# Kernel optimization log

Hardware: AMD Instinct MI355X
Metric: run time of the kernel (lower is better)

Reference implementation:

```python
import jax, jax.numpy as jnp
import numpy as np

N_NODES = 100000
N_EDGES = 1600000
N_FEAT = 128
HIDDEN = 128
OUT = 1
NUM_GRAPHS = 2048


def setup_inputs() -> dict:
    key = jax.random.key(0)
    ks = jax.random.split(key, 8)
    x = jax.random.normal(ks[0], (N_NODES, N_FEAT), dtype=jnp.float32)
    edge_index = jax.random.randint(ks[1], (2, N_EDGES), 0, N_NODES, dtype=jnp.int64)
    batch = jnp.sort(jax.random.randint(ks[2], (N_NODES,), 0, NUM_GRAPHS, dtype=jnp.int64))
    s = 1.0 / np.sqrt(N_FEAT)
    W1 = jax.random.normal(ks[3], (N_FEAT, HIDDEN), dtype=jnp.float32) * s
    b1 = jnp.zeros((HIDDEN,), dtype=jnp.float32)
    W2 = jax.random.normal(ks[4], (HIDDEN, HIDDEN), dtype=jnp.float32) * s
    b2 = jnp.zeros((HIDDEN,), dtype=jnp.float32)
    Wlin = jax.random.normal(ks[5], (HIDDEN, OUT), dtype=jnp.float32) * s
    blin = jnp.zeros((OUT,), dtype=jnp.float32)
    return {"x": x, "edge_index": edge_index, "batch": batch,
            "W1": W1, "b1": b1, "W2": W2, "b2": b2, "Wlin": Wlin, "blin": blin}


def gcn_conv(x, W, b, src, dst, n_nodes):
    # PyG GCNConv: x' = D^{-1/2} (A + I) D^{-1/2} (X W) + b, deg includes self-loop
    xw = x @ W  # [N, H]
    deg = jax.ops.segment_sum(jnp.ones(src.shape[0], xw.dtype), dst, num_segments=n_nodes) + 1.0
    dinv = jax.lax.rsqrt(deg)
    norm = dinv[src] * dinv[dst]  # [E]
    agg = jax.ops.segment_sum(xw[src] * norm[:, None], dst, num_segments=n_nodes)
    # self-loop contribution: norm = deg^{-1}
    return agg + xw * (1.0 / deg)[:, None] + b


def global_mean_pool(x, batch, num_graphs):
    sums = jax.ops.segment_sum(x, batch, num_segments=num_graphs)
    cnts = jax.ops.segment_sum(jnp.ones(x.shape[0], x.dtype), batch, num_segments=num_graphs)
    return sums / jnp.maximum(cnts, 1.0)[:, None]


def reference(x, edge_index, batch, W1, b1, W2, b2, Wlin, blin):
    src, dst = edge_index[0], edge_index[1]
    n = x.shape[0]
    h = gcn_conv(x, W1, b1, src, dst, n)
    h = jax.nn.relu(h)  # dropout is a no-op in eval mode
    h = gcn_conv(h, W2, b2, src, dst, n)
    g = global_mean_pool(h, batch, NUM_GRAPHS)  # [G, H]
    return g @ Wlin + blin
```

## Files before the change

### kernel.cpp

```cpp
#include <hip/hip_runtime.h>

#define N_NODES   100000
#define N_EDGES   1600000
#define NFEAT     128
#define NGRAPHS   2048
#define CBSHIFT   7
#define BSZ       128
#define NCB       ((N_NODES + BSZ - 1) / BSZ)
#define N_META    (NCB * BSZ)
#define CAP       2432
#define P1_EPB    4096
#define P1_BLOCKS ((N_EDGES + P1_EPB - 1) / P1_EPB)
#define GEMM_HALF   391
#define G1_BLOCKS 2048
#define G2_BLOCKS ((4 * N_NODES + 255) / 256)
#define ZCNT      (NGRAPHS + NCB)
#define ZB        ((ZCNT + 255) / 256)
#define MISC_BLOCKS (17 + ZB + 8)

typedef __attribute__((ext_vector_type(8))) short short8;
typedef __attribute__((ext_vector_type(4))) float f32x4;

__device__ __forceinline__ unsigned short f2bf(float f) {
    unsigned int u = __float_as_uint(f);
    u += 0x7FFFu + ((u >> 16) & 1u);
    return (unsigned short)(u >> 16);
}

__device__ __forceinline__ void acc8s(float* acc, uint4 v, float s) {
    acc[0] = fmaf(s, __uint_as_float(v.x << 16), acc[0]);
    acc[1] = fmaf(s, __uint_as_float(v.x & 0xFFFF0000u), acc[1]);
    acc[2] = fmaf(s, __uint_as_float(v.y << 16), acc[2]);
    acc[3] = fmaf(s, __uint_as_float(v.y & 0xFFFF0000u), acc[3]);
    acc[4] = fmaf(s, __uint_as_float(v.z << 16), acc[4]);
    acc[5] = fmaf(s, __uint_as_float(v.z & 0xFFFF0000u), acc[5]);
    acc[6] = fmaf(s, __uint_as_float(v.w << 16), acc[6]);
    acc[7] = fmaf(s, __uint_as_float(v.w & 0xFFFF0000u), acc[7]);
}

__device__ __forceinline__ void gemm_tile(const float* __restrict__ X,
                                          const unsigned short* __restrict__ WT,
                                          unsigned short* __restrict__ C,
                                          int gblk, int tid) {
    const int R0   = gblk * 128;
    const int wv   = tid >> 6;
    const int lane = tid & 63;
    const int m16  = lane & 15;
    const int quad = lane >> 4;
    const int r0 = R0 + wv * 32 + m16;
    const int r1 = r0 + 16;
    const bool ok0 = r0 < N_NODES, ok1 = r1 < N_NODES;

    f32x4 acc[2][8] = {};
    #pragma unroll
    for (int ks = 0; ks < 4; ++ks) {
        const int k0 = ks * 32 + quad * 8;
        short8 a0 = {}, a1 = {};
        if (ok0) {
            float4 f0 = *(const float4*)(X + (size_t)r0 * NFEAT + k0);
            float4 f1 = *(const float4*)(X + (size_t)r0 * NFEAT + k0 + 4);
            a0[0] = (short)f2bf(f0.x); a0[1] = (short)f2bf(f0.y);
            a0[2] = (short)f2bf(f0.z); a0[3] = (short)f2bf(f0.w);
            a0[4] = (short)f2bf(f1.x); a0[5] = (short)f2bf(f1.y);
            a0[6] = (short)f2bf(f1.z); a0[7] = (short)f2bf(f1.w);
        }
        if (ok1) {
            float4 f0 = *(const float4*)(X + (size_t)r1 * NFEAT + k0);
            float4 f1 = *(const float4*)(X + (size_t)r1 * NFEAT + k0 + 4);
            a1[0] = (short)f2bf(f0.x); a1[1] = (short)f2bf(f0.y);
            a1[2] = (short)f2bf(f0.z); a1[3] = (short)f2bf(f0.w);
            a1[4] = (short)f2bf(f1.x); a1[5] = (short)f2bf(f1.y);
            a1[6] = (short)f2bf(f1.z); a1[7] = (short)f2bf(f1.w);
        }
        #pragma unroll
        for (int ct = 0; ct < 8; ++ct) {
            short8 bb = *(const short8*)(WT + (ct * 16 + m16) * 128 + k0);
            acc[0][ct] = __builtin_amdgcn_mfma_f32_16x16x32_bf16(a0, bb, acc[0][ct], 0, 0, 0);
            acc[1][ct] = __builtin_amdgcn_mfma_f32_16x16x32_bf16(a1, bb, acc[1][ct], 0, 0, 0);
        }
    }
    #pragma unroll
    for (int t2 = 0; t2 < 2; ++t2) {
        int rbase = R0 + wv * 32 + t2 * 16 + quad * 4;
        #pragma unroll
        for (int reg = 0; reg < 4; ++reg) {
            int gr = rbase + reg;
            if (gr < N_NODES) {
                short8 v;
                #pragma unroll
                for (int ct = 0; ct < 8; ++ct)
                    v[ct] = (short)f2bf(acc[t2][ct][reg]);
                *(short8*)(C + (size_t)gr * NFEAT + m16 * 8) = v;
            }
        }
    }
}

__global__ __launch_bounds__(256) void k_misc(const float* __restrict__ W1,
                                              unsigned short* __restrict__ WT1,
                                              const float* __restrict__ W2,
                                              const float* __restrict__ Wlin,
                                              const float* __restrict__ b2,
                                              const float* __restrict__ blin,
                                              float* __restrict__ w2l,
                                              int* __restrict__ zeros,
                                              const int* __restrict__ batch,
                                              float* __restrict__ cntf) {
    const int blk = blockIdx.x;
    const int t = threadIdx.x;
    if (blk < 16) {
        int base = blk * 1024 + t * 4;
        #pragma unroll
        for (int q = 0; q < 4; ++q) {
            int i = base + q;
            int n = i >> 7, k = i & 127;
            WT1[i] = f2bf(W1[k * 128 + n]);
        }
    } else if (blk == 16) {
        __shared__ float s[256];
        int i = t >> 1, half = t & 1;
        float ps = 0.f;
        for (int j = half * 64; j < half * 64 + 64; ++j)
            ps += W2[i * 128 + j] * Wlin[j];
        s[t] = ps;
        __syncthreads();
        if (!half) w2l[i] = s[t] + s[t + 1];
        __syncthreads();
        float pc = (t < 128) ? b2[t] * Wlin[t] : 0.f;
        s[t] = pc;
        __syncthreads();
        for (int off = 128; off > 0; off >>= 1) {
            if (t < off) s[t] += s[t + off];
            __syncthreads();
        }
        if (t == 0) w2l[128] = s[0] + blin[0];
    } else if (blk < 17 + ZB) {
        int i = (blk - 17) * 256 + t;
        if (i < ZCNT) zeros[i] = 0;
    } else {
        int g = (blk - (17 + ZB)) * 256 + t;
        int lo = 0, hi = N_NODES;
        while (lo < hi) { int m = (lo + hi) >> 1; if (batch[m] < g) lo = m + 1; else hi = m; }
        int lb = lo;
        lo = 0; hi = N_NODES;
        int g1 = g + 1;
        while (lo < hi) { int m = (lo + hi) >> 1; if (batch[m] < g1) lo = m + 1; else hi = m; }
        cntf[g] = fmaxf((float)(lo - lb), 1.0f);
    }
}

__global__ __launch_bounds__(256) void k_gA_p1(const float* __restrict__ X,
                                               const unsigned short* __restrict__ WT,
                                               unsigned short* __restrict__ C,
                                               const int* __restrict__ src,
                                               const int* __restrict__ dst,
                                               int* __restrict__ bcur,
                                               unsigned int* __restrict__ pairs) {
    if (blockIdx.x < GEMM_HALF) {
        gemm_tile(X, WT, C, blockIdx.x, threadIdx.x);
        return;
    }
    const int b = blockIdx.x - GEMM_HALF;
    __shared__ int hist[NCB], base[NCB], cur[NCB];
    const int t = threadIdx.x;
    for (int i = t; i < NCB; i += 256) { hist[i] = 0; cur[i] = 0; }
    __syncthreads();
    const int e0 = b * P1_EPB;
    const int e1 = min(e0 + P1_EPB, N_EDGES);
    const int q0 = e0 >> 2, q1 = e1 >> 2;
    const int4* dst4 = (const int4*)dst;
    const int4* src4 = (const int4*)src;
    for (int q = q0 + t; q < q1; q += 256) {
        int4 d4 = dst4[q];
        atomicAdd(&hist[d4.x >> CBSHIFT], 1);
        atomicAdd(&hist[d4.y >> CBSHIFT], 1);
        atomicAdd(&hist[d4.z >> CBSHIFT], 1);
        atomicAdd(&hist[d4.w >> CBSHIFT], 1);
    }
    __syncthreads();
    const int off0 = (b * 89) % NCB;
    for (int k = t; k < NCB; k += 256) {
        int i = k + off0;
        if (i >= NCB) i -= NCB;
        int c = hist[i];
        base[i] = c ? (i * CAP + atomicAdd(&bcur[i], c)) : 0;
    }
    __syncthreads();
    for (int q = q0 + t; q < q1; q += 256) {
        int4 d4 = dst4[q];
        int4 s4 = src4[q];
        #pragma unroll
        for (int u = 0; u < 4; ++u) {
            int d = (u == 0) ? d4.x : (u == 1) ? d4.y : (u == 2) ? d4.z : d4.w;
            int sv = (u == 0) ? s4.x : (u == 1) ? s4.y : (u == 2) ? s4.z : s4.w;
            int bb = d >> CBSHIFT;
            int r = atomicAdd(&cur[bb], 1);
            int idx = base[bb] + r;
            if (idx < (bb + 1) * CAP)
                pairs[idx] = (unsigned int)sv | ((unsigned int)(d & (BSZ - 1)) << 17);
        }
    }
}

__global__ __launch_bounds__(256) void k_gB_p2(const float* __restrict__ X,
                                               const unsigned short* __restrict__ WT,
                                               unsigned short* __restrict__ C,
                                               const unsigned int* __restrict__ pairs,
                                               const int* __restrict__ bcur,
                                               int* __restrict__ csr_src,
                                               float* __restrict__ dinv,
                                               int4* __restrict__ meta,
                                               int2* __restrict__ nm) {
    if (blockIdx.x < GEMM_HALF) {
        gemm_tile(X, WT, C, blockIdx.x + GEMM_HALF, threadIdx.x);
        return;
    }
    const int b = blockIdx.x - GEMM_HALF;
    __shared__ int hist[BSZ], sst[BSZ], cur[BSZ], s[BSZ], dh[64], dhc[64];
    const int t = threadIdx.x;
    const int cnt_b = min(bcur[b], CAP);
    const int beg = b * CAP;
    const int end = beg + cnt_b;
    const int end4 = beg + (cnt_b & ~3);
    if (t < BSZ) { hist[t] = 0; cur[t] = 0; }
    if (t < 64) { dh[t] = 0; dhc[t] = 0; }
    __syncthreads();
    for (int i = beg + 4 * t; i < end4; i += 1024) {
        uint4 pv = *(const uint4*)(pairs + i);
        atomicAdd(&hist[pv.x >> 17], 1);
        atomicAdd(&hist[pv.y >> 17], 1);
        atomicAdd(&hist[pv.z >> 17], 1);
        atomicAdd(&hist[pv.w >> 17], 1);
    }
    for (int i = end4 + t; i < end; i += 256)
        atomicAdd(&hist[pairs[i] >> 17], 1);
    __syncthreads();
    int v = (t < BSZ) ? hist[t] : 0;
    if (t < BSZ) s[t] = v;
    __syncthreads();
    for (int off = 1; off < BSZ; off <<= 1) {
        int x = (t >= off && t < BSZ) ? s[t - off] : 0;
        __syncthreads();
        if (t < BSZ) s[t] += x;
        __syncthreads();
    }
    if (t < BSZ) sst[t] = s[t] - v;
    __syncthreads();
    const int node = (b << CBSHIFT) + t;
    const bool valid = (t < BSZ) && (node < N_NODES);
    if (valid) {
        dinv[node] = rsqrtf((float)v + 1.0f);
        nm[node] = make_int2(beg + sst[t], v);
        atomicAdd(&dh[63 - min(v, 63)], 1);
    }
    for (int i = beg + 4 * t; i < end4; i += 1024) {
        uint4 pv = *(const uint4*)(pairs + i);
        #pragma unroll
        for (int u = 0; u < 4; ++u) {
            unsigned int p = (u == 0) ? pv.x : (u == 1) ? pv.y : (u == 2) ? pv.z : pv.w;
            int dl = p >> 17;
            int r = atomicAdd(&cur[dl], 1);
            csr_src[beg + sst[dl] + r] = (int)(p & 0x1FFFFu);
        }
    }
    for (int i = end4 + t; i < end; i += 256) {
        unsigned int pv = pairs[i];
        int dl = pv >> 17;
        int r = atomicAdd(&cur[dl], 1);
        csr_src[beg + sst[dl] + r] = (int)(pv & 0x1FFFFu);
    }
    __syncthreads();
    if (t < 64) s[t] = dh[t];
    __syncthreads();
    for (int off = 1; off < 64; off <<= 1) {
        int x = (t >= off && t < 64) ? s[t - off] : 0;
        __syncthreads();
        if (t < 64) s[t] += x;
        __syncthreads();
    }
    if (valid) {
        int bin = 63 - min(v, 63);
        int r = atomicAdd(&dhc[bin], 1);
        int rank = s[bin] - dh[bin] + r;
        meta[(size_t)rank * NCB + b] =
            make_int4(beg + sst[t], v, __float_as_int(rsqrtf((float)v + 1.0f)), node);
    } else if (t < BSZ) {
        meta[(size_t)t * NCB + b] = make_int4(0, 0, 0, -1);
    }
}

__global__ __launch_bounds__(256) void k_gather1(const unsigned short* __restrict__ xwb,
                                                 const int* __restrict__ csr_src,
                                                 const float* __restrict__ dinv,
                                                 const float* __restrict__ b,
                                                 const float* __restrict__ w2l,
                                                 const int4* __restrict__ meta,
                                                 float* __restrict__ z) {
    const int t     = threadIdx.x;
    const int lane  = t & 63;
    const int p     = lane & 15;
    const int gbase = lane & 48;
    const int j0    = p & 7;
    const int ngroups = G1_BLOCKS * 16;
    int gid = blockIdx.x * 16 + (t >> 4);
    const uint4* tab = (const uint4*)xwb;
    float bl[8], wl[8];
    #pragma unroll
    for (int j = 0; j < 8; ++j) { bl[j] = b[16 * j + p]; wl[j] = w2l[16 * j + p]; }

    for (int nidx = gid; nidx < N_META; nidx += ngroups) {
        const int4 md = meta[nidx];
        const int node  = md.w;
        if (node < 0) continue;
        const int beg   = md.x;
        const int cnt   = md.y;
        const float dvn = __int_as_float(md.z);
        float acc[8] = {};
        acc8s(acc, tab[(size_t)node * 16 + p], dvn);
        const int nch = (cnt + 7) >> 3;
        if (nch) {
            int myA; float dvA; uint4 vA[8];
            int myB; float dvB; uint4 vB[8];
            {
                bool vld = j0 < cnt;
                int jj = vld ? j0 : 0;
                int sld = csr_src[beg + jj];
                myA = vld ? sld : node;
                float dv = dinv[myA];
                dvA = vld ? dv : 0.f;
                #pragma unroll
                for (int q = 0; q < 8; ++q) {
                    int idx = __shfl(myA, gbase + q);
                    vA[q] = tab[(size_t)idx * 16 + p];
                }
            }
            int c = 0;
            for (;;) {
                const bool hb = (c + 1 < nch);
                if (hb) {
                    int j = (c + 1) * 8 + j0;
                    bool vld = j < cnt;
                    int jj = vld ? j : 0;
                    int sld = csr_src[beg + jj];
                    myB = vld ? sld : node;
                    float dv = dinv[myB];
                    dvB = vld ? dv : 0.f;
                    #pragma unroll
                    for (int q = 0; q < 8; ++q) {
                        int idx = __shfl(myB, gbase + q);
                        vB[q] = tab[(size_t)idx * 16 + p];
                    }
                }
                #pragma unroll
                for (int q = 0; q < 8; ++q) {
                    float sv = __shfl(dvA, gbase + q);
                    acc8s(acc, vA[q], sv);
                }
                ++c;
                if (!hb) break;
                const bool ha = (c + 1 < nch);
                if (ha) {
                    int j = (c + 1) * 8 + j0;
                    bool vld = j < cnt;
                    int jj = vld ? j : 0;
                    int sld = csr_src[beg + jj];
                    myA = vld ? sld : node;
                    float dv = dinv[myA];
                    dvA = vld ? dv : 0.f;
                    #pragma unroll
                    for (int q = 0; q < 8; ++q) {
                        int idx = __shfl(myA, gbase + q);
                        vA[q] = tab[(size_t)idx * 16 + p];
                    }
                }
                #pragma unroll
                for (int q = 0; q < 8; ++q) {
                    float sv = __shfl(dvB, gbase + q);
                    acc8s(acc, vB[q], sv);
                }
                ++c;
                if (!ha) break;
            }
        }
        float s = 0.f;
        #pragma unroll
        for (int j = 0; j < 8; ++j)
            s = fmaf(fmaxf(fmaf(acc[j], dvn, bl[j]), 0.f), wl[j], s);
        s += __shfl_xor(s, 1);
        s += __shfl_xor(s, 2);
        s += __shfl_xor(s, 4);
        s += __shfl_xor(s, 8);
        if (p == 0) z[node] = s * dvn;
    }
}

__global__ __launch_bounds__(256) void k_g2(const float* __restrict__ z,
                                            const int* __restrict__ csr_src,
                                            const int2* __restrict__ nm,
                                            const float* __restrict__ dinv,
                                            const int* __restrict__ batch,
                                            float* __restrict__ gsum) {
    __shared__ float lgs[64];
    __shared__ int sg0;
    const int t = threadIdx.x;
    if (t < 64) lgs[t] = 0.f;
    const int node0 = blockIdx.x * 64;
    if (t == 0) sg0 = batch[node0];
    __syncthreads();
    const int g0 = sg0;
    const int node = node0 + (t >> 2);
    const int q = t & 3;
    if (node < N_NODES) {
        int2 m = nm[node];
        const int beg = m.x, cnt = m.y;
        float a = (q == 0) ? z[node] : 0.f;
        for (int j = q; j < cnt; j += 4)
            a += z[csr_src[beg + j]];
        a += __shfl_xor(a, 1);
        a += __shfl_xor(a, 2);
        if (q == 0) {
            float val = a * dinv[node];
            int rel = batch[node] - g0;
            if (rel < 64) atomicAdd(&lgs[rel], val);
            else atomicAdd(&gsum[batch[node]], val);
        }
    }
    __syncthreads();
    if (t < 64 && lgs[t] != 0.f) atomicAdd(&gsum[g0 + t], lgs[t]);
}

__global__ void k_final(const float* __restrict__ gsum, const float* __restrict__ cntf,
                        const float* __restrict__ c2, float* __restrict__ out) {
    int g = blockIdx.x * blockDim.x + threadIdx.x;
    if (g >= NGRAPHS) return;
    out[g] = gsum[g] / cntf[g] + c2[0];
}

extern "C" void kernel_launch(void* const* d_in, const int* in_sizes, int n_in,
                              void* d_out, int out_size, void* d_ws, size_t ws_size,
                              hipStream_t stream) {
    const float* x    = (const float*)d_in[0];
    const int*   ei   = (const int*)d_in[1];
    const int*   bat  = (const int*)d_in[2];
    const float* W1   = (const float*)d_in[3];
    const float* b1   = (const float*)d_in[4];
    const float* W2   = (const float*)d_in[5];
    const float* b2   = (const float*)d_in[6];
    const float* Wlin = (const float*)d_in[7];
    const float* blin = (const float*)d_in[8];
    float* out = (float*)d_out;

    const int* src = ei;
    const int* dst = ei + N_EDGES;

    const size_t NF = (size_t)N_NODES * NFEAT;
    unsigned short* bufA = (unsigned short*)d_ws;
    float* z       = (float*)(bufA + NF);
    float* dinv    = z + N_NODES;
    float* gsum    = dinv + N_NODES;
    int* bcur      = (int*)(gsum + NGRAPHS);
    float* cntf    = (float*)(bcur + NCB);
    unsigned short* WT1 = (unsigned short*)(cntf + NGRAPHS);
    float* w2l     = (float*)(WT1 + 128 * 128);
    unsigned int* pairs = (unsigned int*)(w2l + 132);
    int* csr_src   = (int*)(pairs + (size_t)NCB * CAP);
    int4* meta     = (int4*)(((size_t)(csr_src + (size_t)NCB * CAP) + 15) & ~(size_t)15);
    int2* nm       = (int2*)(meta + N_META);

    const int BS = 256;

    k_misc<<<MISC_BLOCKS, BS, 0, stream>>>(W1, WT1, W2, Wlin, b2, blin, w2l,
                                           (int*)gsum, bat, cntf);
    k_gA_p1<<<GEMM_HALF + P1_BLOCKS, BS, 0, stream>>>(x, WT1, bufA, src, dst, bcur, pairs);
    k_gB_p2<<<GEMM_HALF + NCB, BS, 0, stream>>>(x, WT1, bufA, pairs, bcur, csr_src,
                                                dinv, meta, nm);
    k_gather1<<<G1_BLOCKS, BS, 0, stream>>>(bufA, csr_src, dinv, b1, w2l, meta, z);
    k_g2<<<G2_BLOCKS, BS, 0, stream>>>(z, csr_src, nm, dinv, bat, gsum);
    k_final<<<(NGRAPHS + BS - 1) / BS, BS, 0, stream>>>(gsum, cntf, w2l + 128, out);
}
```

Measured before the change: 228.9 us.

## Fuse CSR bucket scatter into layer-1 gather with LDS-resident CSR

The CSR scatter and degree-ordered rank metadata move out of the GEMM/degree kernel into a new per-bucket kernel. That kernel builds the bucket's CSR slice in shared memory, sorts its nodes by degree locally, and immediately runs the layer-1 gather from the LDS copy. This removes the global meta array and the reread of csr_src in the gather. The cost is that gather parallelism is now tied to one block per 128-node bucket, which may hurt load balance compared with the old global degree-sorted grid-stride schedule. Shared-memory use per block also rises, which may lower occupancy.

```diff
diff --git a/kernel.cpp b/kernel.cpp
--- a/kernel.cpp
+++ b/kernel.cpp
@@ -7,12 +7,10 @@
 #define CBSHIFT   7
 #define BSZ       128
 #define NCB       ((N_NODES + BSZ - 1) / BSZ)
-#define N_META    (NCB * BSZ)
 #define CAP       2432
 #define P1_EPB    4096
 #define P1_BLOCKS ((N_EDGES + P1_EPB - 1) / P1_EPB)
 #define GEMM_HALF   391
-#define G1_BLOCKS 2048
 #define G2_BLOCKS ((4 * N_NODES + 255) / 256)
 #define ZCNT      (NGRAPHS + NCB)
 #define ZB        ((ZCNT + 255) / 256)
@@ -202,28 +200,25 @@
     }
 }
 
-__global__ __launch_bounds__(256) void k_gB_p2(const float* __restrict__ X,
-                                               const unsigned short* __restrict__ WT,
-                                               unsigned short* __restrict__ C,
-                                               const unsigned int* __restrict__ pairs,
-                                               const int* __restrict__ bcur,
-                                               int* __restrict__ csr_src,
-                                               float* __restrict__ dinv,
-                                               int4* __restrict__ meta,
-                                               int2* __restrict__ nm) {
+__global__ __launch_bounds__(256) void k_gB_deg(const float* __restrict__ X,
+                                                const unsigned short* __restrict__ WT,
+                                                unsigned short* __restrict__ C,
+                                                const unsigned int* __restrict__ pairs,
+                                                const int* __restrict__ bcur,
+                                                int2* __restrict__ nm,
+                                                float* __restrict__ dinv) {
     if (blockIdx.x < GEMM_HALF) {
         gemm_tile(X, WT, C, blockIdx.x + GEMM_HALF, threadIdx.x);
         return;
     }
     const int b = blockIdx.x - GEMM_HALF;
-    __shared__ int hist[BSZ], sst[BSZ], cur[BSZ], s[BSZ], dh[64], dhc[64];
+    __shared__ int hist[BSZ], s[BSZ];
     const int t = threadIdx.x;
     const int cnt_b = min(bcur[b], CAP);
     const int beg = b * CAP;
     const int end = beg + cnt_b;
     const int end4 = beg + (cnt_b & ~3);
-    if (t < BSZ) { hist[t] = 0; cur[t] = 0; }
-    if (t < 64) { dh[t] = 0; dhc[t] = 0; }
+    if (t < BSZ) hist[t] = 0;
     __syncthreads();
     for (int i = beg + 4 * t; i < end4; i += 1024) {
         uint4 pv = *(const uint4*)(pairs + i);
@@ -244,77 +239,89 @@
         if (t < BSZ) s[t] += x;
         __syncthreads();
     }
-    if (t < BSZ) sst[t] = s[t] - v;
-    __syncthreads();
     const int node = (b << CBSHIFT) + t;
-    const bool valid = (t < BSZ) && (node < N_NODES);
+    if (t < BSZ && node < N_NODES) {
+        nm[node] = make_int2(beg + s[t] - v, v);
+        dinv[node] = rsqrtf((float)v + 1.0f);
+    }
+}
+
+__global__ __launch_bounds__(256) void k_bg(const unsigned short* __restrict__ xwb,
+                                            const unsigned int* __restrict__ pairs,
+                                            const int* __restrict__ bcur,
+                                            const int2* __restrict__ nm,
+                                            const float* __restrict__ dinv,
+                                            const float* __restrict__ b,
+                                            const float* __restrict__ w2l,
+                                            int* __restrict__ csr_src,
+                                            float* __restrict__ z) {
+    __shared__ int csr_lds[CAP];
+    __shared__ int begL[BSZ], cntL[BSZ], cur[BSZ];
+    __shared__ float dvL[BSZ];
+    __shared__ int dh[64], dhc[64], s64[64];
+    __shared__ unsigned char rankord[BSZ];
+    const int bb = blockIdx.x;
+    const int t = threadIdx.x;
+    const int node0 = bb << CBSHIFT;
+    if (t < BSZ) {
+        int node = node0 + t;
+        cur[t] = 0;
+        rankord[t] = 255;
+        if (node < N_NODES) {
+            int2 m = nm[node];
+            begL[t] = m.x - bb * CAP;
+            cntL[t] = m.y;
+            dvL[t] = dinv[node];
+        } else { begL[t] = 0; cntL[t] = 0; dvL[t] = 0.f; }
+    }
+    if (t < 64) { dh[t] = 0; dhc[t] = 0; }
+    __syncthreads();
+    const bool valid = (t < BSZ) && (node0 + t < N_NODES);
+    int bin = 0;
+    if (valid) { bin = 63 - min(cntL[t], 63); atomicAdd(&dh[bin], 1); }
+    __syncthreads();
+    if (t < 64) s64[t] = dh[t];
+    __syncthreads();
+    for (int off = 1; off < 64; off <<= 1) {
+        int x = (t >= off && t < 64) ? s64[t - off] : 0;
+        __syncthreads();
+        if (t < 64) s64[t] += x;
+        __syncthreads();
+    }
     if (valid) {
-        dinv[node] = rsqrtf((float)v + 1.0f);
-        nm[node] = make_int2(beg + sst[t], v);
-        atomicAdd(&dh[63 - min(v, 63)], 1);
-    }
-    for (int i = beg + 4 * t; i < end4; i += 1024) {
-        uint4 pv = *(const uint4*)(pairs + i);
-        #pragma unroll
-        for (int u = 0; u < 4; ++u) {
-            unsigned int p = (u == 0) ? pv.x : (u == 1) ? pv.y : (u == 2) ? pv.z : pv.w;
-            int dl = p >> 17;
-            int r = atomicAdd(&cur[dl], 1);
-            csr_src[beg + sst[dl] + r] = (int)(p & 0x1FFFFu);
-        }
-    }
-    for (int i = end4 + t; i < end; i += 256) {
-        unsigned int pv = pairs[i];
+        int r = atomicAdd(&dhc[bin], 1);
+        rankord[s64[bin] - dh[bin] + r] = (unsigned char)t;
+    }
+    const int cnt_b = min(bcur[bb], CAP);
+    const int pbase = bb * CAP;
+    __syncthreads();
+    for (int i = t; i < cnt_b; i += 256) {
+        unsigned int pv = pairs[pbase + i];
         int dl = pv >> 17;
         int r = atomicAdd(&cur[dl], 1);
-        csr_src[beg + sst[dl] + r] = (int)(pv & 0x1FFFFu);
-    }
-    __syncthreads();
-    if (t < 64) s[t] = dh[t];
-    __syncthreads();
-    for (int off = 1; off < 64; off <<= 1) {
-        int x = (t >= off && t < 64) ? s[t - off] : 0;
-        __syncthreads();
-        if (t < 64) s[t] += x;
-        __syncthreads();
-    }
-    if (valid) {
-        int bin = 63 - min(v, 63);
-        int r = atomicAdd(&dhc[bin], 1);
-        int rank = s[bin] - dh[bin] + r;
-        meta[(size_t)rank * NCB + b] =
-            make_int4(beg + sst[t], v, __float_as_int(rsqrtf((float)v + 1.0f)), node);
-    } else if (t < BSZ) {
-        meta[(size_t)t * NCB + b] = make_int4(0, 0, 0, -1);
-    }
-}
-
-__global__ __launch_bounds__(256) void k_gather1(const unsigned short* __restrict__ xwb,
-                                                 const int* __restrict__ csr_src,
-                                                 const float* __restrict__ dinv,
-                                                 const float* __restrict__ b,
-                                                 const float* __restrict__ w2l,
-                                                 const int4* __restrict__ meta,
-                                                 float* __restrict__ z) {
-    const int t     = threadIdx.x;
+        int idx = begL[dl] + r;
+        int sv = (int)(pv & 0x1FFFFu);
+        csr_lds[idx] = sv;
+        csr_src[pbase + idx] = sv;
+    }
+    __syncthreads();
     const int lane  = t & 63;
     const int p     = lane & 15;
     const int gbase = lane & 48;
     const int j0    = p & 7;
-    const int ngroups = G1_BLOCKS * 16;
-    int gid = blockIdx.x * 16 + (t >> 4);
+    const int grp   = t >> 4;
     const uint4* tab = (const uint4*)xwb;
     float bl[8], wl[8];
     #pragma unroll
     for (int j = 0; j < 8; ++j) { bl[j] = b[16 * j + p]; wl[j] = w2l[16 * j + p]; }
 
-    for (int nidx = gid; nidx < N_META; nidx += ngroups) {
-        const int4 md = meta[nidx];
-        const int node  = md.w;
-        if (node < 0) continue;
-        const int beg   = md.x;
-        const int cnt   = md.y;
-        const float dvn = __int_as_float(md.z);
+    for (int r = grp; r < BSZ; r += 16) {
+        const int tl = rankord[r];
+        if (tl == 255) continue;
+        const int node  = node0 + tl;
+        const int begl  = begL[tl];
+        const int cnt   = cntL[tl];
+        const float dvn = dvL[tl];
         float acc[8] = {};
         acc8s(acc, tab[(size_t)node * 16 + p], dvn);
         const int nch = (cnt + 7) >> 3;
@@ -324,7 +331,7 @@
             {
                 bool vld = j0 < cnt;
                 int jj = vld ? j0 : 0;
-                int sld = csr_src[beg + jj];
+                int sld = csr_lds[begl + jj];
                 myA = vld ? sld : node;
                 float dv = dinv[myA];
                 dvA = vld ? dv : 0.f;
@@ -341,7 +348,7 @@
                     int j = (c + 1) * 8 + j0;
                     bool vld = j < cnt;
                     int jj = vld ? j : 0;
-                    int sld = csr_src[beg + jj];
+                    int sld = csr_lds[begl + jj];
                     myB = vld ? sld : node;
                     float dv = dinv[myB];
                     dvB = vld ? dv : 0.f;
@@ -363,7 +370,7 @@
                     int j = (c + 1) * 8 + j0;
                     bool vld = j < cnt;
                     int jj = vld ? j : 0;
-                    int sld = csr_src[beg + jj];
+                    int sld = csr_lds[begl + jj];
                     myA = vld ? sld : node;
                     float dv = dinv[myA];
                     dvA = vld ? dv : 0.f;
@@ -464,17 +471,15 @@
     float* w2l     = (float*)(WT1 + 128 * 128);
     unsigned int* pairs = (unsigned int*)(w2l + 132);
     int* csr_src   = (int*)(pairs + (size_t)NCB * CAP);
-    int4* meta     = (int4*)(((size_t)(csr_src + (size_t)NCB * CAP) + 15) & ~(size_t)15);
-    int2* nm       = (int2*)(meta + N_META);
+    int2* nm       = (int2*)(csr_src + (size_t)NCB * CAP);
 
     const int BS = 256;
 
     k_misc<<<MISC_BLOCKS, BS, 0, stream>>>(W1, WT1, W2, Wlin, b2, blin, w2l,
                                            (int*)gsum, bat, cntf);
     k_gA_p1<<<GEMM_HALF + P1_BLOCKS, BS, 0, stream>>>(x, WT1, bufA, src, dst, bcur, pairs);
-    k_gB_p2<<<GEMM_HALF + NCB, BS, 0, stream>>>(x, WT1, bufA, pairs, bcur, csr_src,
-                                                dinv, meta, nm);
-    k_gather1<<<G1_BLOCKS, BS, 0, stream>>>(bufA, csr_src, dinv, b1, w2l, meta, z);
+    k_gB_deg<<<GEMM_HALF + NCB, BS, 0, stream>>>(x, WT1, bufA, pairs, bcur, nm, dinv);
+    k_bg<<<NCB, BS, 0, stream>>>(bufA, pairs, bcur, nm, dinv, b1, w2l, csr_src, z);
     k_g2<<<G2_BLOCKS, BS, 0, stream>>>(z, csr_src, nm, dinv, bat, gsum);
     k_final<<<(NGRAPHS + BS - 1) / BS, BS, 0, stream>>>(gsum, cntf, w2l + 128, out);
 }
```

Result: slower. 239.8 us (+4.8%).
